# Optimization experiments

Measured on AMD Instinct MI355X. Metric: run time of the kernel, lower is better.

## Reference

```python
import jax, jax.numpy as jnp
import numpy as np

EMBED_DIM = 768
Q_DIM = 64
V_DIM = 64
WINDOW_SIZE = 3


def setup_inputs() -> dict:
    key = jax.random.key(0)
    ks = jax.random.split(key, 7)
    B, N = 4, 4096
    s = 1.0 / np.sqrt(EMBED_DIM)
    x = jax.random.normal(ks[0], (B, N, EMBED_DIM), dtype=jnp.float32)
    Wq = jax.random.normal(ks[1], (EMBED_DIM, Q_DIM), dtype=jnp.float32) * s
    bq = jax.random.normal(ks[2], (Q_DIM,), dtype=jnp.float32) * 0.01
    Wk = jax.random.normal(ks[3], (EMBED_DIM, Q_DIM), dtype=jnp.float32) * s
    bk = jax.random.normal(ks[4], (Q_DIM,), dtype=jnp.float32) * 0.01
    Wv = jax.random.normal(ks[5], (EMBED_DIM, V_DIM), dtype=jnp.float32) * s
    bv = jax.random.normal(ks[6], (V_DIM,), dtype=jnp.float32) * 0.01
    return {"x": x, "Wq": Wq, "bq": bq, "Wk": Wk, "bk": bk, "Wv": Wv, "bv": bv}


def reference(x, Wq, bq, Wk, bk, Wv, bv):
    # Faithful translation of SliddingWindowAttention.forward, including the
    # original's quirk: diagonal scores are written into columns 0..window_size-1
    # of a full (B, N, N) zero matrix, softmax is taken over ALL N columns
    # (zeros included), and the result is matmul'd with V.
    B, N, _ = x.shape
    Q = x @ Wq + bq  # (B, N, Q_DIM)
    K = x @ Wk + bk  # (B, N, Q_DIM)
    V = x @ Wv + bv  # (B, N, V_DIM)

    half = WINDOW_SIZE // 2
    columns = jnp.zeros((B, N, N), dtype=x.dtype)
    for idx, di in enumerate(range(-half, half + 1)):
        # diagonal offset di: pair row i with column j = i + di (valid rows only)
        rows = np.arange(max(0, -di), N - max(0, di))
        cols_j = rows + di
        c = jnp.einsum('bid,bid->bi', Q[:, rows, :], K[:, cols_j, :])
        columns = columns.at[:, rows, idx].set(c)

    attn = jax.nn.softmax(columns, axis=2)  # (B, N, N)
    return attn @ V  # (B, N, V_DIM)
```

## Files before the change

kernel.cpp:

```cpp
#include <hip/hip_runtime.h>
#include <math.h>

#define EMBED 768
#define NTOK  4096
#define NB    4
#define ROWS  16384
#define CN    192

typedef __attribute__((ext_vector_type(8))) short bf16x8;
typedef __attribute__((ext_vector_type(4))) float f32x4;

__device__ inline void split2(float f, short& h, short& l) {
  union { float f; unsigned u; } a; a.f = f;
  unsigned r = (a.u + 0x7FFFu + ((a.u >> 16) & 1u)) & 0xFFFF0000u;
  h = (short)(r >> 16);
  union { unsigned u; float f; } hf; hf.u = r;
  union { float f; unsigned u; } b; b.f = f - hf.f;
  l = (short)((b.u + 0x7FFFu + ((b.u >> 16) & 1u)) >> 16);
}

__global__ __launch_bounds__(256) void wprep(const float* __restrict__ Wq,
                                             const float* __restrict__ Wk,
                                             const float* __restrict__ Wv,
                                             unsigned short* __restrict__ Wt) {
  int t = blockIdx.x * 256 + threadIdx.x;
  int n = t / 768, k = t - n * 768;
  float w;
  if (n < 64)        w = Wq[k * 64 + n];
  else if (n < 128)  w = Wk[k * 64 + (n - 64)];
  else               w = Wv[k * 64 + (n - 128)];
  short h, l; split2(w, h, l);
  Wt[(size_t)n * 768 + k]         = (unsigned short)h;
  Wt[(size_t)(192 + n) * 768 + k] = (unsigned short)l;
}

__global__ __launch_bounds__(128) void qkv_mfma(const float* __restrict__ x,
                                                const unsigned short* __restrict__ Wtu,
                                                const float* __restrict__ bq,
                                                const float* __restrict__ bk,
                                                const float* __restrict__ bv,
                                                float* __restrict__ C) {
  const int lane = threadIdx.x & 63;
  const int wn   = threadIdx.x >> 6;
  const int ml   = lane & 15;
  const int q    = lane >> 4;
  const int r0   = blockIdx.x * 32;
  const int nbase = wn * 96;

  f32x4 acc[2][6] = {};

  const float* xa0 = x + (size_t)(r0 + ml) * EMBED + q * 8;
  const float* xa1 = x + (size_t)(r0 + 16 + ml) * EMBED + q * 8;
  const bf16x8* wt = (const bf16x8*)Wtu;

  int bidx[12];
#pragma unroll
  for (int p = 0; p < 2; ++p)
#pragma unroll
    for (int nt = 0; nt < 6; ++nt)
      bidx[p * 6 + nt] = (p * 192 + nbase + nt * 16 + ml) * 96 + q;

  float4 ca[4]; bf16x8 cb[12];
  ca[0] = *(const float4*)(xa0);     ca[1] = *(const float4*)(xa0 + 4);
  ca[2] = *(const float4*)(xa1);     ca[3] = *(const float4*)(xa1 + 4);
#pragma unroll
  for (int j = 0; j < 12; ++j) cb[j] = wt[bidx[j]];

  for (int ks = 0; ks < 24; ++ks) {
    float4 na[4]; bf16x8 nb[12];
    if (ks < 23) {
      const float* p0 = xa0 + (ks + 1) * 32;
      const float* p1 = xa1 + (ks + 1) * 32;
      na[0] = *(const float4*)(p0);  na[1] = *(const float4*)(p0 + 4);
      na[2] = *(const float4*)(p1);  na[3] = *(const float4*)(p1 + 4);
#pragma unroll
      for (int j = 0; j < 12; ++j) nb[j] = wt[bidx[j] + (ks + 1) * 4];
    }

    bf16x8 ah0, al0, ah1, al1;
    {
      float f0[8] = {ca[0].x, ca[0].y, ca[0].z, ca[0].w,
                     ca[1].x, ca[1].y, ca[1].z, ca[1].w};
      float f1[8] = {ca[2].x, ca[2].y, ca[2].z, ca[2].w,
                     ca[3].x, ca[3].y, ca[3].z, ca[3].w};
#pragma unroll
      for (int j = 0; j < 8; ++j) {
        short h, l;
        split2(f0[j], h, l); ah0[j] = h; al0[j] = l;
        split2(f1[j], h, l); ah1[j] = h; al1[j] = l;
      }
    }

#pragma unroll
    for (int nt = 0; nt < 6; ++nt) {
      bf16x8 bh = cb[nt], bl = cb[6 + nt];
      acc[0][nt] = __builtin_amdgcn_mfma_f32_16x16x32_bf16(ah0, bh, acc[0][nt], 0, 0, 0);
      acc[0][nt] = __builtin_amdgcn_mfma_f32_16x16x32_bf16(ah0, bl, acc[0][nt], 0, 0, 0);
      acc[0][nt] = __builtin_amdgcn_mfma_f32_16x16x32_bf16(al0, bh, acc[0][nt], 0, 0, 0);
      acc[1][nt] = __builtin_amdgcn_mfma_f32_16x16x32_bf16(ah1, bh, acc[1][nt], 0, 0, 0);
      acc[1][nt] = __builtin_amdgcn_mfma_f32_16x16x32_bf16(ah1, bl, acc[1][nt], 0, 0, 0);
      acc[1][nt] = __builtin_amdgcn_mfma_f32_16x16x32_bf16(al1, bh, acc[1][nt], 0, 0, 0);
    }

#pragma unroll
    for (int j = 0; j < 4; ++j)  ca[j] = na[j];
#pragma unroll
    for (int j = 0; j < 12; ++j) cb[j] = nb[j];
  }

#pragma unroll
  for (int nt = 0; nt < 6; ++nt) {
    int n = nbase + nt * 16 + ml;
    float bias = (n < 64) ? bq[n] : (n < 128) ? bk[n - 64] : bv[n - 128];
#pragma unroll
    for (int mt = 0; mt < 2; ++mt) {
#pragma unroll
      for (int reg = 0; reg < 4; ++reg) {
        int row = r0 + mt * 16 + q * 4 + reg;
        C[(size_t)row * CN + n] = acc[mt][nt][reg] + bias;
      }
    }
  }
}

__global__ __launch_bounds__(256) void vsum_kernel(const float* __restrict__ C,
                                                   float* __restrict__ Vsum) {
  __shared__ float red[4][64];
  const int t = threadIdx.x;
  const int d = t & 63;
  const int g = t >> 6;
  const int batch = blockIdx.x >> 6;
  const int chunk = blockIdx.x & 63;
  const size_t base =
      ((size_t)batch * NTOK + (size_t)chunk * 64 + (size_t)g * 16) * CN + 128 + d;
  float s = 0.f;
#pragma unroll
  for (int rr = 0; rr < 16; ++rr) s += C[base + (size_t)rr * CN];
  red[g][d] = s;
  __syncthreads();
  if (g == 0) {
    atomicAdd(&Vsum[batch * 64 + d],
              red[0][d] + red[1][d] + red[2][d] + red[3][d]);
  }
}

__global__ __launch_bounds__(256) void attn_kernel(const float* __restrict__ C,
                                                   const float* __restrict__ Vsum,
                                                   float* __restrict__ out) {
  const int t    = threadIdx.x;
  const int lane = t & 63;
  const int wave = t >> 6;
  const int r = blockIdx.x * 4 + wave;
  const int b = r >> 12;
  const int i = r & (NTOK - 1);

  const float q  = C[(size_t)r * CN + lane];
  const float kc = C[(size_t)r * CN + 64 + lane];
  float km = 0.f, kp = 0.f;
  if (i > 0)        km = C[(size_t)(r - 1) * CN + 64 + lane];
  if (i < NTOK - 1) kp = C[(size_t)(r + 1) * CN + 64 + lane];

  float p0 = q * km, p1 = q * kc, p2 = q * kp;
#pragma unroll
  for (int off = 32; off > 0; off >>= 1) {
    p0 += __shfl_xor(p0, off, 64);
    p1 += __shfl_xor(p1, off, 64);
    p2 += __shfl_xor(p2, off, 64);
  }

  const float s0 = (i > 0) ? p0 : 0.f;
  const float s1 = p1;
  const float s2 = (i < NTOK - 1) ? p2 : 0.f;
  const float m  = fmaxf(fmaxf(s0, s1), fmaxf(s2, 0.f));
  const float e0 = expf(s0 - m);
  const float e1 = expf(s1 - m);
  const float e2 = expf(s2 - m);
  const float ez = expf(-m);
  const float Z  = e0 + e1 + e2 + (float)(NTOK - 3) * ez;

  const size_t vb = ((size_t)b * NTOK) * CN + 128;
  const float v0 = C[vb + lane];
  const float v1 = C[vb + CN + lane];
  const float v2 = C[vb + 2 * (size_t)CN + lane];
  const float vs = Vsum[b * 64 + lane];

  out[(size_t)r * 64 + lane] =
      (e0 * v0 + e1 * v1 + e2 * v2 + ez * (vs - v0 - v1 - v2)) / Z;
}

extern "C" void kernel_launch(void* const* d_in, const int* in_sizes, int n_in,
                              void* d_out, int out_size, void* d_ws, size_t ws_size,
                              hipStream_t stream) {
  const float* x  = (const float*)d_in[0];
  const float* Wq = (const float*)d_in[1];
  const float* bq = (const float*)d_in[2];
  const float* Wk = (const float*)d_in[3];
  const float* bk = (const float*)d_in[4];
  const float* Wv = (const float*)d_in[5];
  const float* bv = (const float*)d_in[6];
  float* out = (float*)d_out;

  float* C    = (float*)d_ws;
  float* Vsum = C + (size_t)ROWS * CN;
  unsigned short* Wt = (unsigned short*)(Vsum + NB * 64);

  hipMemsetAsync(Vsum, 0, NB * 64 * sizeof(float), stream);
  wprep<<<576, 256, 0, stream>>>(Wq, Wk, Wv, Wt);
  qkv_mfma<<<512, 128, 0, stream>>>(x, Wt, bq, bk, bv, C);
  vsum_kernel<<<256, 256, 0, stream>>>(C, Vsum);
  attn_kernel<<<ROWS / 4, 256, 0, stream>>>(C, Vsum, out);
}
```

Baseline: 149.6 us.

## Split QKV GEMM across six waves and use packed bf16 split conversions

The QKV projection block grows from 2 waves (96 columns each) to 6 waves (32 columns each), with launch bounds (384,3). This cuts per-wave accumulator and register use so more waves can hide memory latency, but every wave now reloads the same x rows and redoes their hi/lo bf16 split, so x loads and conversion work per block triple. The manual rounding bit-trick is replaced with packed HIP bf16 intrinsics, and the weight prep is re-indexed so consecutive threads read contiguous weights.

```diff
diff --git a/kernel.cpp b/kernel.cpp
--- a/kernel.cpp
+++ b/kernel.cpp
@@ -1,4 +1,5 @@
 #include <hip/hip_runtime.h>
+#include <hip/hip_bf16.h>
 #include <math.h>
 
 #define EMBED 768
@@ -9,14 +10,34 @@
 
 typedef __attribute__((ext_vector_type(8))) short bf16x8;
 typedef __attribute__((ext_vector_type(4))) float f32x4;
-
-__device__ inline void split2(float f, short& h, short& l) {
-  union { float f; unsigned u; } a; a.f = f;
-  unsigned r = (a.u + 0x7FFFu + ((a.u >> 16) & 1u)) & 0xFFFF0000u;
-  h = (short)(r >> 16);
-  union { unsigned u; float f; } hf; hf.u = r;
-  union { float f; unsigned u; } b; b.f = f - hf.f;
-  l = (short)((b.u + 0x7FFFu + ((b.u >> 16) & 1u)) >> 16);
+typedef __attribute__((ext_vector_type(4))) unsigned int u32x4;
+
+__device__ inline void split8(const float4& a0, const float4& a1,
+                              bf16x8& h, bf16x8& l) {
+  const float f[8] = {a0.x, a0.y, a0.z, a0.w, a1.x, a1.y, a1.z, a1.w};
+  u32x4 hw, lw;
+#pragma unroll
+  for (int j = 0; j < 4; ++j) {
+    float2 p = make_float2(f[2 * j], f[2 * j + 1]);
+    __hip_bfloat162 hb = __float22bfloat162_rn(p);
+    float2 hf = __bfloat1622float2(hb);
+    __hip_bfloat162 lb =
+        __float22bfloat162_rn(make_float2(p.x - hf.x, p.y - hf.y));
+    union { __hip_bfloat162 b; unsigned u; } cu, cl;
+    cu.b = hb; cl.b = lb;
+    hw[j] = cu.u; lw[j] = cl.u;
+  }
+  h = __builtin_bit_cast(bf16x8, hw);
+  l = __builtin_bit_cast(bf16x8, lw);
+}
+
+__device__ inline void split1(float f, unsigned short& h, unsigned short& l) {
+  __hip_bfloat16 hb = __float2bfloat16(f);
+  float hf = __bfloat162float(hb);
+  __hip_bfloat16 lb = __float2bfloat16(f - hf);
+  union { __hip_bfloat16 b; unsigned short u; } a, b2;
+  a.b = hb; b2.b = lb;
+  h = a.u; l = b2.u;
 }
 
 __global__ __launch_bounds__(256) void wprep(const float* __restrict__ Wq,
@@ -24,102 +45,100 @@
                                              const float* __restrict__ Wv,
                                              unsigned short* __restrict__ Wt) {
   int t = blockIdx.x * 256 + threadIdx.x;
-  int n = t / 768, k = t - n * 768;
+  int k = t / CN, c = t - k * CN;
   float w;
-  if (n < 64)        w = Wq[k * 64 + n];
-  else if (n < 128)  w = Wk[k * 64 + (n - 64)];
-  else               w = Wv[k * 64 + (n - 128)];
-  short h, l; split2(w, h, l);
-  Wt[(size_t)n * 768 + k]         = (unsigned short)h;
-  Wt[(size_t)(192 + n) * 768 + k] = (unsigned short)l;
-}
-
-__global__ __launch_bounds__(128) void qkv_mfma(const float* __restrict__ x,
-                                                const unsigned short* __restrict__ Wtu,
-                                                const float* __restrict__ bq,
-                                                const float* __restrict__ bk,
-                                                const float* __restrict__ bv,
-                                                float* __restrict__ C) {
+  if (c < 64)        w = Wq[k * 64 + c];
+  else if (c < 128)  w = Wk[k * 64 + (c - 64)];
+  else               w = Wv[k * 64 + (c - 128)];
+  unsigned short h, l; split1(w, h, l);
+  Wt[(size_t)c * EMBED + k]          = h;
+  Wt[(size_t)(CN + c) * EMBED + k]   = l;
+}
+
+__global__ __launch_bounds__(384, 3) void qkv_mfma(
+    const float* __restrict__ x, const unsigned short* __restrict__ Wtu,
+    const float* __restrict__ bq, const float* __restrict__ bk,
+    const float* __restrict__ bv, float* __restrict__ C) {
   const int lane = threadIdx.x & 63;
   const int wn   = threadIdx.x >> 6;
   const int ml   = lane & 15;
-  const int q    = lane >> 4;
+  const int qd   = lane >> 4;
   const int r0   = blockIdx.x * 32;
-  const int nbase = wn * 96;
-
-  f32x4 acc[2][6] = {};
-
-  const float* xa0 = x + (size_t)(r0 + ml) * EMBED + q * 8;
-  const float* xa1 = x + (size_t)(r0 + 16 + ml) * EMBED + q * 8;
+  const int n0   = wn * 32;
+
+  f32x4 acc[2][2] = {};
+
+  const float* xa0 = x + (size_t)(r0 + ml) * EMBED + qd * 8;
+  const float* xa1 = x + (size_t)(r0 + 16 + ml) * EMBED + qd * 8;
   const bf16x8* wt = (const bf16x8*)Wtu;
 
-  int bidx[12];
-#pragma unroll
-  for (int p = 0; p < 2; ++p)
-#pragma unroll
-    for (int nt = 0; nt < 6; ++nt)
-      bidx[p * 6 + nt] = (p * 192 + nbase + nt * 16 + ml) * 96 + q;
-
-  float4 ca[4]; bf16x8 cb[12];
-  ca[0] = *(const float4*)(xa0);     ca[1] = *(const float4*)(xa0 + 4);
-  ca[2] = *(const float4*)(xa1);     ca[3] = *(const float4*)(xa1 + 4);
-#pragma unroll
-  for (int j = 0; j < 12; ++j) cb[j] = wt[bidx[j]];
+  int bidx[2][2];
+#pragma unroll
+  for (int pl = 0; pl < 2; ++pl)
+#pragma unroll
+    for (int nt = 0; nt < 2; ++nt)
+      bidx[pl][nt] = (pl * CN + n0 + nt * 16 + ml) * 96 + qd;
+
+  float4 ca[2][2];
+  bf16x8 cb[2][2];
+  ca[0][0] = *(const float4*)(xa0);  ca[0][1] = *(const float4*)(xa0 + 4);
+  ca[1][0] = *(const float4*)(xa1);  ca[1][1] = *(const float4*)(xa1 + 4);
+#pragma unroll
+  for (int pl = 0; pl < 2; ++pl)
+#pragma unroll
+    for (int nt = 0; nt < 2; ++nt) cb[pl][nt] = wt[bidx[pl][nt]];
 
   for (int ks = 0; ks < 24; ++ks) {
-    float4 na[4]; bf16x8 nb[12];
+    float4 na[2][2]; bf16x8 nb[2][2];
     if (ks < 23) {
       const float* p0 = xa0 + (ks + 1) * 32;
       const float* p1 = xa1 + (ks + 1) * 32;
-      na[0] = *(const float4*)(p0);  na[1] = *(const float4*)(p0 + 4);
-      na[2] = *(const float4*)(p1);  na[3] = *(const float4*)(p1 + 4);
-#pragma unroll
-      for (int j = 0; j < 12; ++j) nb[j] = wt[bidx[j] + (ks + 1) * 4];
+      na[0][0] = *(const float4*)(p0);  na[0][1] = *(const float4*)(p0 + 4);
+      na[1][0] = *(const float4*)(p1);  na[1][1] = *(const float4*)(p1 + 4);
+      const int ko = (ks + 1) * 4;
+#pragma unroll
+      for (int pl = 0; pl < 2; ++pl)
+#pragma unroll
+        for (int nt = 0; nt < 2; ++nt) nb[pl][nt] = wt[bidx[pl][nt] + ko];
     }
 
-    bf16x8 ah0, al0, ah1, al1;
-    {
-      float f0[8] = {ca[0].x, ca[0].y, ca[0].z, ca[0].w,
-                     ca[1].x, ca[1].y, ca[1].z, ca[1].w};
-      float f1[8] = {ca[2].x, ca[2].y, ca[2].z, ca[2].w,
-                     ca[3].x, ca[3].y, ca[3].z, ca[3].w};
-#pragma unroll
-      for (int j = 0; j < 8; ++j) {
-        short h, l;
-        split2(f0[j], h, l); ah0[j] = h; al0[j] = l;
-        split2(f1[j], h, l); ah1[j] = h; al1[j] = l;
+    bf16x8 ah[2], al[2];
+    split8(ca[0][0], ca[0][1], ah[0], al[0]);
+    split8(ca[1][0], ca[1][1], ah[1], al[1]);
+
+#pragma unroll
+    for (int mt = 0; mt < 2; ++mt)
+#pragma unroll
+      for (int nt = 0; nt < 2; ++nt) {
+        acc[mt][nt] = __builtin_amdgcn_mfma_f32_16x16x32_bf16(
+            al[mt], cb[0][nt], acc[mt][nt], 0, 0, 0);
+        acc[mt][nt] = __builtin_amdgcn_mfma_f32_16x16x32_bf16(
+            ah[mt], cb[1][nt], acc[mt][nt], 0, 0, 0);
+        acc[mt][nt] = __builtin_amdgcn_mfma_f32_16x16x32_bf16(
+            ah[mt], cb[0][nt], acc[mt][nt], 0, 0, 0);
       }
+
+#pragma unroll
+    for (int mt = 0; mt < 2; ++mt) {
+      ca[mt][0] = na[mt][0]; ca[mt][1] = na[mt][1];
     }
-
-#pragma unroll
-    for (int nt = 0; nt < 6; ++nt) {
-      bf16x8 bh = cb[nt], bl = cb[6 + nt];
-      acc[0][nt] = __builtin_amdgcn_mfma_f32_16x16x32_bf16(ah0, bh, acc[0][nt], 0, 0, 0);
-      acc[0][nt] = __builtin_amdgcn_mfma_f32_16x16x32_bf16(ah0, bl, acc[0][nt], 0, 0, 0);
-      acc[0][nt] = __builtin_amdgcn_mfma_f32_16x16x32_bf16(al0, bh, acc[0][nt], 0, 0, 0);
-      acc[1][nt] = __builtin_amdgcn_mfma_f32_16x16x32_bf16(ah1, bh, acc[1][nt], 0, 0, 0);
-      acc[1][nt] = __builtin_amdgcn_mfma_f32_16x16x32_bf16(ah1, bl, acc[1][nt], 0, 0, 0);
-      acc[1][nt] = __builtin_amdgcn_mfma_f32_16x16x32_bf16(al1, bh, acc[1][nt], 0, 0, 0);
-    }
-
-#pragma unroll
-    for (int j = 0; j < 4; ++j)  ca[j] = na[j];
-#pragma unroll
-    for (int j = 0; j < 12; ++j) cb[j] = nb[j];
-  }
-
-#pragma unroll
-  for (int nt = 0; nt < 6; ++nt) {
-    int n = nbase + nt * 16 + ml;
+#pragma unroll
+    for (int pl = 0; pl < 2; ++pl)
+#pragma unroll
+      for (int nt = 0; nt < 2; ++nt) cb[pl][nt] = nb[pl][nt];
+  }
+
+#pragma unroll
+  for (int nt = 0; nt < 2; ++nt) {
+    int n = n0 + nt * 16 + ml;
     float bias = (n < 64) ? bq[n] : (n < 128) ? bk[n - 64] : bv[n - 128];
 #pragma unroll
-    for (int mt = 0; mt < 2; ++mt) {
+    for (int mt = 0; mt < 2; ++mt)
 #pragma unroll
       for (int reg = 0; reg < 4; ++reg) {
-        int row = r0 + mt * 16 + q * 4 + reg;
+        int row = r0 + mt * 16 + qd * 4 + reg;
         C[(size_t)row * CN + n] = acc[mt][nt][reg] + bias;
       }
-    }
   }
 }
 
@@ -206,7 +225,7 @@
 
   hipMemsetAsync(Vsum, 0, NB * 64 * sizeof(float), stream);
   wprep<<<576, 256, 0, stream>>>(Wq, Wk, Wv, Wt);
-  qkv_mfma<<<512, 128, 0, stream>>>(x, Wt, bq, bk, bv, C);
+  qkv_mfma<<<512, 384, 0, stream>>>(x, Wt, bq, bk, bv, C);
   vsum_kernel<<<256, 256, 0, stream>>>(C, Vsum);
   attn_kernel<<<ROWS / 4, 256, 0, stream>>>(C, Vsum, out);
 }
```

After: 169.5 us. 13.3% more time.
